# Performance work log

Measured on AMD Instinct MI355X. Metric: run time of the kernel, lower is better.

The kernel has to match this reference:

```python
import jax, jax.numpy as jnp
import numpy as np
from jax import lax

E = 4; D_MODEL = 128; D_FF = 128; DT_RANK = 32; D_STATE = 16
L = 12; PAD = 12  # padding_factor=1.0 -> pad L extra zeros
K_TOP = 6; U = 1e-6; EPS = 1e-5
BATCH = 8; NODES = 307; BN = BATCH * NODES
FREQ_IN = (L + PAD) // 2 + 1 + K_TOP  # 19
FREQ_OUT = L // 2 + 1                 # 7


def setup_inputs() -> dict:
    key = jax.random.key(0)
    ks = jax.random.split(key, 14)
    x = jax.random.normal(ks[0], (BN, L, D_MODEL), jnp.float32)
    graph = jax.random.normal(ks[1], (BATCH, L, D_FF, D_FF), jnp.float32) * (1.0 / D_FF)
    in_w = jax.random.normal(ks[2], (E, 2 * D_FF, D_MODEL), jnp.float32) * 0.05
    in_b = jax.random.normal(ks[3], (E, 2 * D_FF), jnp.float32) * 0.02
    x_w = jax.random.normal(ks[4], (E, DT_RANK + 2 * D_STATE + D_FF, D_FF), jnp.float32) * 0.05
    dt_w = jax.random.uniform(ks[5], (E, D_FF, DT_RANK), jnp.float32,
                              -(DT_RANK ** -0.5), DT_RANK ** -0.5)
    dt_b = -2.0 + 0.1 * jax.random.normal(ks[6], (E, D_FF), jnp.float32)
    A_log = jnp.broadcast_to(jnp.log(jnp.arange(1, D_STATE + 1, dtype=jnp.float32))[None, None, :],
                             (E, 1, D_STATE))
    out_w = jax.random.normal(ks[7], (E, D_MODEL, D_FF), jnp.float32) * 0.05
    out_b = jax.random.normal(ks[8], (E, D_MODEL), jnp.float32) * 0.02
    fw_r = jax.random.normal(ks[9], (E, FREQ_OUT, FREQ_IN), jnp.float32) * (FREQ_IN ** -0.5)
    fw_i = jax.random.normal(ks[10], (E, FREQ_OUT, FREQ_IN), jnp.float32) * (FREQ_IN ** -0.5)
    norm_w = jnp.ones((E, D_MODEL), jnp.float32)
    blk_w = jnp.full((E,), 0.5, jnp.float32)
    blk_b = jnp.full((E,), 0.5, jnp.float32)
    return dict(x=x, graph=graph, in_w=in_w, in_b=in_b, x_w=x_w, dt_w=dt_w, dt_b=dt_b,
                A_log=A_log, out_w=out_w, out_b=out_b, fw_r=fw_r, fw_i=fw_i,
                norm_w=norm_w, blk_w=blk_w, blk_b=blk_b)


def _rmsnorm(x, w):
    return x * lax.rsqrt(jnp.mean(x * x, axis=-1, keepdims=True) + EPS) * w


def _mamba_block(x, graph, in_w, in_b, x_w, dt_w, dt_b, A_log, out_w, out_b, fw_r, fw_i):
    bn, Ls, d = x.shape
    # --- FFT frequency gating ---
    x_padded = jnp.concatenate([x, jnp.zeros((bn, PAD, d), x.dtype)], axis=1)
    fp = jnp.fft.rfft(x_padded, axis=1)          # [bn, 13, d] complex
    f = jnp.fft.rfft(x, axis=1)                  # [bn, 7, d] complex
    sq_adj = (f.real + U) ** 2 + (f.imag + U) ** 2
    fs = -jnp.sort(-sq_adj, axis=1)[:, :K_TOP]   # top-K along freq dim, descending
    cat = jnp.concatenate([fp, fs.astype(fp.dtype)], axis=1)  # [bn, 19, d]
    W = lax.complex(fw_r, fw_i)                  # [7, 19]
    freq_proj = jnp.einsum('bkd,ok->bod', cat, W)  # [bn, 7, d]
    wf = jax.nn.softmax(freq_proj.real ** 2 + freq_proj.imag ** 2, axis=2)
    x_freq = jnp.fft.irfft(wf * f, axis=1)       # [bn, 12, d] (n = 2*(7-1))
    # --- input projection ---
    xz = x @ in_w.T + in_b
    xs, z = jnp.split(xz, 2, axis=-1)
    xs = jax.nn.silu(xs)
    # --- SSM ---
    A = -jnp.exp(A_log.astype(jnp.float32))      # [1, d_state]
    dbcd = xs @ x_w.T
    delta, B, C, Dp = jnp.split(dbcd, [DT_RANK, DT_RANK + D_STATE, DT_RANK + 2 * D_STATE], axis=-1)
    delta = jax.nn.softplus(delta @ dt_w.T + dt_b)  # [bn, L, d_ff]
    # graph mixing over nodes: bn = batch * n
    batch = graph.shape[0]
    delta = delta.reshape(batch, -1, Ls, D_FF)
    delta = jnp.einsum('bnsd,bsda->bnsa', delta, graph).reshape(bn, Ls, D_FF)
    deltaA = jnp.exp(delta[..., None] * A)             # [bn, L, d_ff, d_state]
    BX = delta[..., None] * B[:, :, None, :] * xs[..., None]
    dA_t = jnp.moveaxis(deltaA, 1, 0)
    bx_t = jnp.moveaxis(BX, 1, 0)

    def step(h, ab):
        dA, bx = ab
        h = dA * h + bx
        return h, h

    h0 = jnp.zeros((bn, D_FF, D_STATE), xs.dtype)
    _, hs = lax.scan(step, h0, (dA_t, bx_t))
    hs = jnp.moveaxis(hs, 0, 1)                        # [bn, L, d_ff, d_state]
    y = jnp.einsum('blds,bls->bld', hs, C) + Dp * xs
    # --- gate + output ---
    out = y * jax.nn.silu(z) * x_freq
    return out @ out_w.T + out_b


def reference(x, graph, in_w, in_b, x_w, dt_w, dt_b, A_log, out_w, out_b,
              fw_r, fw_i, norm_w, blk_w, blk_b):
    for i in range(E):
        xn = _rmsnorm(x, norm_w[i])
        out = _mamba_block(xn, graph, in_w[i], in_b[i], x_w[i], dt_w[i], dt_b[i],
                           A_log[i], out_w[i], out_b[i], fw_r[i], fw_i[i])
        out = blk_w[i] * out + blk_b[i]
        x = x + out  # dropout is identity in eval
    return jax.nn.silu(x)
```

## Files before the change

kernel.cpp:

```cpp
#include <hip/hip_runtime.h>
#include <math.h>

#define BN    2456
#define LSEQ  12
#define DM    128
#define NODES 307
#define MROWS 29472

typedef __bf16 bfx8 __attribute__((ext_vector_type(8)));
typedef float  f32x4 __attribute__((ext_vector_type(4)));

#define MFMA16(a, b, c) __builtin_amdgcn_mfma_f32_16x16x32_bf16(a, b, c, 0, 0, 0)

__device__ __forceinline__ float fsilu(float v)     { return v / (1.0f + __expf(-v)); }
__device__ __forceinline__ float fsoftplus(float x) { return fmaxf(x, 0.f) + __logf(1.0f + __expf(-fabsf(x))); }

__global__ __launch_bounds__(256)
void k_convert(const float* __restrict__ in_w, const float* __restrict__ x_w,
               const float* __restrict__ out_w, const float* __restrict__ dt_w,
               const float* __restrict__ graph,
               __bf16* __restrict__ in_w_bf, __bf16* __restrict__ x_w_bf,
               __bf16* __restrict__ out_w_bf, __bf16* __restrict__ dtw_bf,
               __bf16* __restrict__ graphT_bf) {
    int idx = blockIdx.x * 256 + threadIdx.x;
    if (idx < 131072) { in_w_bf[idx] = (__bf16)in_w[idx]; return; }
    idx -= 131072;
    if (idx < 98304) { x_w_bf[idx] = (__bf16)x_w[idx]; return; }
    idx -= 98304;
    if (idx < 65536) { out_w_bf[idx] = (__bf16)out_w[idx]; return; }
    idx -= 65536;
    if (idx < 65536) { dtw_bf[idx] = (__bf16)dt_w[idx]; return; }
    idx -= 65536;
    if (idx < 1572864) {
        int bl = idx >> 14, r = idx & 16383;
        int d = r >> 7, a = r & 127;
        graphT_bf[(size_t)bl * 16384 + a * 128 + d] = (__bf16)graph[idx];
    }
}

template <int N>
__device__ __forceinline__ void red_sum128(float* v, float* sred, int tid) {
#pragma unroll
    for (int off = 32; off; off >>= 1)
#pragma unroll
        for (int i = 0; i < N; ++i) v[i] += __shfl_xor(v[i], off, 64);
    if ((tid & 63) == 0) {
#pragma unroll
        for (int i = 0; i < N; ++i) sred[(tid >> 6) * N + i] = v[i];
    }
    __syncthreads();
#pragma unroll
    for (int i = 0; i < N; ++i) v[i] = sred[i] + sred[N + i];
    __syncthreads();
}

template <int N>
__device__ __forceinline__ void red_max128(float* v, float* sred, int tid) {
#pragma unroll
    for (int off = 32; off; off >>= 1)
#pragma unroll
        for (int i = 0; i < N; ++i) v[i] = fmaxf(v[i], __shfl_xor(v[i], off, 64));
    if ((tid & 63) == 0) {
#pragma unroll
        for (int i = 0; i < N; ++i) sred[(tid >> 6) * N + i] = v[i];
    }
    __syncthreads();
#pragma unroll
    for (int i = 0; i < N; ++i) v[i] = fmaxf(sred[i], sred[N + i]);
    __syncthreads();
}

__global__ __launch_bounds__(128)
void k_freq(const float* __restrict__ xcur, const float* __restrict__ norm_w,
            const float* __restrict__ fw_r, const float* __restrict__ fw_i,
            __bf16* __restrict__ xn_bf, __bf16* __restrict__ xfq_bf, int e) {
    __shared__ float s_c[24], s_s[24], s_wr[133], s_wi[133];
    __shared__ float sred[24];
    const int row = blockIdx.x, tid = threadIdx.x;
    const int b = row / NODES, n = row - b * NODES;

    if (tid < 24) {
        float sv, cv;
        __sincosf(6.283185307179586f * (float)tid / 24.0f, &sv, &cv);
        s_c[tid] = cv; s_s[tid] = sv;
    }
    for (int i = tid; i < 133; i += 128) { s_wr[i] = fw_r[e * 133 + i]; s_wi[i] = fw_i[e * 133 + i]; }

    const float* xp = xcur + (size_t)row * 1536 + tid;
    float xv[12], v[12];
#pragma unroll
    for (int l = 0; l < 12; ++l) { xv[l] = xp[l * 128]; v[l] = xv[l] * xv[l]; }
    __syncthreads();
    red_sum128<12>(v, sred, tid);

    const float nrmw = norm_w[e * DM + tid];
    float xnr[12];
#pragma unroll
    for (int l = 0; l < 12; ++l)
        xnr[l] = xv[l] * rsqrtf(v[l] * (1.0f / 128.0f) + 1e-5f) * nrmw;

#pragma unroll
    for (int l = 0; l < 12; ++l)
        xn_bf[((size_t)(b * 12 + l) * NODES + n) * 128 + tid] = (__bf16)xnr[l];

    float fpr[13], fpi[13];
#pragma unroll
    for (int k = 0; k < 13; ++k) { fpr[k] = 0.f; fpi[k] = 0.f; }
#pragma unroll
    for (int l = 0; l < 12; ++l) {
#pragma unroll
        for (int k = 0; k < 13; ++k) {
            const int t = (k * l) % 24;
            fpr[k] += xnr[l] * s_c[t];
            fpi[k] -= xnr[l] * s_s[t];
        }
    }

    float a7[7];
#pragma unroll
    for (int o2 = 0; o2 < 7; ++o2) {
        float ar = fpr[2 * o2] + 1e-6f, ai = fpi[2 * o2] + 1e-6f;
        a7[o2] = ar * ar + ai * ai;
    }
#pragma unroll
    for (int pss = 0; pss < 6; ++pss)
#pragma unroll
        for (int j = 0; j < 6; ++j) {
            float hi = fmaxf(a7[j], a7[j + 1]);
            float lo = fminf(a7[j], a7[j + 1]);
            a7[j] = hi; a7[j + 1] = lo;
        }

    float p7[7];
#pragma unroll
    for (int o2 = 0; o2 < 7; ++o2) {
        float pr = 0.f, pi = 0.f;
#pragma unroll
        for (int k = 0; k < 13; ++k) {
            const float wr = s_wr[o2 * 19 + k], wi = s_wi[o2 * 19 + k];
            pr += fpr[k] * wr - fpi[k] * wi;
            pi += fpr[k] * wi + fpi[k] * wr;
        }
#pragma unroll
        for (int k = 0; k < 6; ++k) {
            const float wr = s_wr[o2 * 19 + 13 + k], wi = s_wi[o2 * 19 + 13 + k];
            pr += a7[k] * wr;
            pi += a7[k] * wi;
        }
        p7[o2] = pr * pr + pi * pi;
    }

    float m7[7], ex[7], sm[7];
#pragma unroll
    for (int o2 = 0; o2 < 7; ++o2) m7[o2] = p7[o2];
    red_max128<7>(m7, sred, tid);
#pragma unroll
    for (int o2 = 0; o2 < 7; ++o2) { ex[o2] = __expf(p7[o2] - m7[o2]); sm[o2] = ex[o2]; }
    red_sum128<7>(sm, sred, tid);

    float gr[7], gi[7];
#pragma unroll
    for (int o2 = 0; o2 < 7; ++o2) {
        const float wf = ex[o2] / sm[o2];
        gr[o2] = wf * fpr[2 * o2];
        gi[o2] = wf * fpi[2 * o2];
    }

#pragma unroll
    for (int l = 0; l < 12; ++l) {
        float val = gr[0] + ((l & 1) ? -gr[6] : gr[6]);
#pragma unroll
        for (int o2 = 1; o2 < 6; ++o2) {
            const int t = (2 * o2 * l) % 24;
            val += 2.0f * (gr[o2] * s_c[t] - gi[o2] * s_s[t]);
        }
        xfq_bf[((size_t)(b * 12 + l) * NODES + n) * 128 + tid] = (__bf16)(val * (1.0f / 12.0f));
    }
}

__global__ __launch_bounds__(256)
void k_fused(const __bf16* __restrict__ xn_bf, const __bf16* __restrict__ in_w_bf,
             const float* __restrict__ in_b, const __bf16* __restrict__ x_w_bf,
             const __bf16* __restrict__ dtw_bf, const float* __restrict__ dt_b,
             const __bf16* __restrict__ graphT_bf,
             __bf16* __restrict__ xs_bf, __bf16* __restrict__ sz_bf,
             float* __restrict__ bcf32, __bf16* __restrict__ dpf,
             __bf16* __restrict__ dmix_bf, int e) {
    __shared__ __bf16 sxs[16 * 136];
    __shared__ __bf16 sdelta[16 * 136];
    __shared__ __bf16 sdel32[16 * 40];
    const int bl = blockIdx.x;
    const int n0 = blockIdx.y * 16;
    const int tid = threadIdx.x;
    const int wave = tid >> 6, lane = tid & 63;
    const int lm = lane & 15, lq = lane >> 4;
    const size_t rowbase = (size_t)bl * NODES + n0;

    const __bf16* Wi = in_w_bf + (size_t)e * 256 * 128;
    const size_t arow = (size_t)bl * NODES + min(n0 + lm, NODES - 1);
    bfx8 af[4];
#pragma unroll
    for (int kc = 0; kc < 4; ++kc)
        af[kc] = *(const bfx8*)(xn_bf + arow * 128 + kc * 32 + lq * 8);

    f32x4 acc[4];
#pragma unroll
    for (int nt = 0; nt < 4; ++nt) acc[nt] = (f32x4){0.f, 0.f, 0.f, 0.f};
#pragma unroll
    for (int kc = 0; kc < 4; ++kc) {
        const int kb = kc * 32 + lq * 8;
#pragma unroll
        for (int ntl = 0; ntl < 4; ++ntl) {
            bfx8 b = *(const bfx8*)(Wi + (size_t)(wave * 64 + ntl * 16 + lm) * 128 + kb);
            acc[ntl] = MFMA16(af[kc], b, acc[ntl]);
        }
    }
#pragma unroll
    for (int ntl = 0; ntl < 4; ++ntl) {
        const int col = wave * 64 + ntl * 16 + lm;
        const float bias = in_b[e * 256 + col];
#pragma unroll
        for (int r = 0; r < 4; ++r) {
            const int node = lq * 4 + r;
            const float v = fsilu(acc[ntl][r] + bias);
            const int ok = (n0 + node) < NODES;
            if (col < 128) {
                sxs[node * 136 + col] = (__bf16)v;
                if (ok) xs_bf[(rowbase + node) * 128 + col] = (__bf16)v;
            } else if (ok) {
                sz_bf[(rowbase + node) * 128 + (col - 128)] = (__bf16)v;
            }
        }
    }
    __syncthreads();

    const __bf16* Wx = x_w_bf + (size_t)e * 192 * 128;
    bfx8 ax[4];
#pragma unroll
    for (int kc = 0; kc < 4; ++kc)
        ax[kc] = *(const bfx8*)(sxs + lm * 136 + kc * 32 + lq * 8);

    f32x4 xacc[3];
#pragma unroll
    for (int nt = 0; nt < 3; ++nt) xacc[nt] = (f32x4){0.f, 0.f, 0.f, 0.f};
#pragma unroll
    for (int kc = 0; kc < 4; ++kc) {
        const int kb = kc * 32 + lq * 8;
#pragma unroll
        for (int ntl = 0; ntl < 3; ++ntl) {
            bfx8 b = *(const bfx8*)(Wx + (size_t)((wave * 3 + ntl) * 16 + lm) * 128 + kb);
            xacc[ntl] = MFMA16(ax[kc], b, xacc[ntl]);
        }
    }
#pragma unroll
    for (int ntl = 0; ntl < 3; ++ntl) {
        const int col = (wave * 3 + ntl) * 16 + lm;
#pragma unroll
        for (int r = 0; r < 4; ++r) {
            const int node = lq * 4 + r;
            const float v = xacc[ntl][r];
            const int ok = (n0 + node) < NODES;
            if (col < 32) sdel32[node * 40 + col] = (__bf16)v;
            else if (col < 64) { if (ok) bcf32[(rowbase + node) * 32 + (col - 32)] = v; }
            else if (ok) dpf[(rowbase + node) * 128 + (col - 64)] = (__bf16)v;
        }
    }
    __syncthreads();

    const __bf16* DW = dtw_bf + (size_t)e * 128 * 32;
    bfx8 ad = *(const bfx8*)(sdel32 + lm * 40 + lq * 8);
    const f32x4 z4 = {0.f, 0.f, 0.f, 0.f};
#pragma unroll
    for (int ntl = 0; ntl < 2; ++ntl) {
        const int nt = wave * 2 + ntl;
        bfx8 b = *(const bfx8*)(DW + (size_t)(nt * 16 + lm) * 32 + lq * 8);
        f32x4 dacc = MFMA16(ad, b, z4);
        const int col = nt * 16 + lm;
        const float bias = dt_b[e * 128 + col];
#pragma unroll
        for (int r = 0; r < 4; ++r) {
            const int node = lq * 4 + r;
            sdelta[node * 136 + col] = (__bf16)fsoftplus(dacc[r] + bias);
        }
    }
    __syncthreads();

    const __bf16* Gp = graphT_bf + (size_t)bl * 16384;
    bfx8 ag[4];
#pragma unroll
    for (int kc = 0; kc < 4; ++kc)
        ag[kc] = *(const bfx8*)(sdelta + lm * 136 + kc * 32 + lq * 8);

#pragma unroll
    for (int ntl = 0; ntl < 2; ++ntl) {
        const int nt = wave * 2 + ntl;
        f32x4 gacc = z4;
#pragma unroll
        for (int kc = 0; kc < 4; ++kc) {
            const int kb = kc * 32 + lq * 8;
            bfx8 b = *(const bfx8*)(Gp + (size_t)(nt * 16 + lm) * 128 + kb);
            gacc = MFMA16(ag[kc], b, gacc);
        }
        const int col = nt * 16 + lm;
#pragma unroll
        for (int r = 0; r < 4; ++r) {
            const int node = lq * 4 + r;
            if ((n0 + node) < NODES)
                dmix_bf[(rowbase + node) * 128 + col] = (__bf16)gacc[r];
        }
    }
}

__global__ __launch_bounds__(128)
void k_scanout(const __bf16* __restrict__ dmix_bf, const __bf16* __restrict__ xs_bf,
               const __bf16* __restrict__ sz_bf, const __bf16* __restrict__ xfq_bf,
               const float* __restrict__ bcf32, const __bf16* __restrict__ dpf,
               const float* __restrict__ A_log, const __bf16* __restrict__ out_w_bf,
               const float* __restrict__ out_b, const float* __restrict__ blk_w,
               const float* __restrict__ blk_b, const float* __restrict__ xprev,
               float* __restrict__ xout, int e, int last) {
    __shared__ __bf16 s_out[16 * 136];
    __shared__ float sBC[384];
    const int row = blockIdx.x, tid = threadIdx.x;
    const int b = row / NODES, n = row - b * NODES;
    for (int i = tid; i < 384; i += 128) {
        const int l = i >> 5, s = i & 31;
        sBC[i] = bcf32[((size_t)(b * 12 + l) * NODES + n) * 32 + s];
    }
    float As[16];
#pragma unroll
    for (int s = 0; s < 16; ++s) As[s] = -__expf(A_log[e * 16 + s]);
#pragma unroll
    for (int r = 12; r < 16; ++r) s_out[r * 136 + tid] = (__bf16)0.f;
    __syncthreads();

    float h[16];
#pragma unroll
    for (int s = 0; s < 16; ++s) h[s] = 0.f;
#pragma unroll
    for (int l = 0; l < 12; ++l) {
        const size_t base = ((size_t)(b * 12 + l) * NODES + n) * 128 + tid;
        const float dl = (float)dmix_bf[base];
        const float xv = (float)xs_bf[base];
        const float Dp = (float)dpf[base];
        const float dlx = dl * xv;
        float y = 0.f;
#pragma unroll
        for (int s = 0; s < 16; ++s) {
            h[s] = __expf(dl * As[s]) * h[s] + sBC[l * 32 + s] * dlx;
            y += h[s] * sBC[l * 32 + 16 + s];
        }
        y += Dp * xv;
        const float g = y * (float)sz_bf[base] * (float)xfq_bf[base];
        s_out[l * 136 + tid] = (__bf16)g;
    }
    __syncthreads();

    const int wave = tid >> 6, lane = tid & 63;
    const int lm = lane & 15, lq = lane >> 4;
    const __bf16* Wo = out_w_bf + (size_t)e * 16384;
    bfx8 a[4];
#pragma unroll
    for (int kc = 0; kc < 4; ++kc)
        a[kc] = *(const bfx8*)(s_out + lm * 136 + kc * 32 + lq * 8);

    f32x4 acc[4];
#pragma unroll
    for (int nt = 0; nt < 4; ++nt) acc[nt] = (f32x4){0.f, 0.f, 0.f, 0.f};
#pragma unroll
    for (int kc = 0; kc < 4; ++kc) {
        const int kb = kc * 32 + lq * 8;
#pragma unroll
        for (int nt = 0; nt < 4; ++nt) {
            bfx8 b = *(const bfx8*)(Wo + (size_t)(wave * 64 + nt * 16 + lm) * 128 + kb);
            acc[nt] = MFMA16(a[kc], b, acc[nt]);
        }
    }

    const float bw = blk_w[e], bb = blk_b[e];
#pragma unroll
    for (int nt = 0; nt < 4; ++nt) {
        const int col = wave * 64 + nt * 16 + lm;
        const float ob = out_b[e * 128 + col];
#pragma unroll
        for (int r = 0; r < 4; ++r) {
            const int m = lq * 4 + r;
            if (m < 12) {
                const size_t gi = ((size_t)row * 12 + m) * 128 + col;
                float v = bw * (acc[nt][r] + ob) + bb + xprev[gi];
                if (last) v = fsilu(v);
                xout[gi] = v;
            }
        }
    }
}

extern "C" void kernel_launch(void* const* d_in, const int* in_sizes, int n_in,
                              void* d_out, int out_size, void* d_ws, size_t ws_size,
                              hipStream_t stream) {
    (void)in_sizes; (void)n_in; (void)out_size; (void)ws_size;
    const float* x_in   = (const float*)d_in[0];
    const float* graph  = (const float*)d_in[1];
    const float* in_w   = (const float*)d_in[2];
    const float* in_b   = (const float*)d_in[3];
    const float* x_w    = (const float*)d_in[4];
    const float* dt_w   = (const float*)d_in[5];
    const float* dt_b   = (const float*)d_in[6];
    const float* A_log  = (const float*)d_in[7];
    const float* out_w  = (const float*)d_in[8];
    const float* out_b  = (const float*)d_in[9];
    const float* fw_r   = (const float*)d_in[10];
    const float* fw_i   = (const float*)d_in[11];
    const float* norm_w = (const float*)d_in[12];
    const float* blk_w  = (const float*)d_in[13];
    const float* blk_b  = (const float*)d_in[14];
    float* out = (float*)d_out;

    float* ws = (float*)d_ws;
    size_t o = 0;
    __bf16* in_w_bf   = (__bf16*)(ws + o); o += 131072 / 2;
    __bf16* x_w_bf    = (__bf16*)(ws + o); o += 98304 / 2;
    __bf16* out_w_bf  = (__bf16*)(ws + o); o += 65536 / 2;
    __bf16* dtw_bf    = (__bf16*)(ws + o); o += 65536 / 2;
    __bf16* graphT_bf = (__bf16*)(ws + o); o += 1572864 / 2;
    const size_t NE = (size_t)MROWS * 128;
    __bf16* xn_bf    = (__bf16*)(ws + o); o += NE / 2;
    __bf16* xfq_bf   = (__bf16*)(ws + o); o += NE / 2;
    __bf16* xs_bf    = (__bf16*)(ws + o); o += NE / 2;
    __bf16* sz_bf    = (__bf16*)(ws + o); o += NE / 2;
    __bf16* dpf      = (__bf16*)(ws + o); o += NE / 2;
    __bf16* dmix_bf  = (__bf16*)(ws + o); o += NE / 2;
    float*  bcf32    = ws + o;            o += (size_t)MROWS * 32;

    hipLaunchKernelGGL(k_convert, dim3(7552), dim3(256), 0, stream,
                       in_w, x_w, out_w, dt_w, graph,
                       in_w_bf, x_w_bf, out_w_bf, dtw_bf, graphT_bf);

    for (int e = 0; e < 4; ++e) {
        const float* xcur = (e == 0) ? x_in : (const float*)out;
        const int last = (e == 3) ? 1 : 0;
        hipLaunchKernelGGL(k_freq, dim3(BN), dim3(128), 0, stream,
                           xcur, norm_w, fw_r, fw_i, xn_bf, xfq_bf, e);
        hipLaunchKernelGGL(k_fused, dim3(96, 20), dim3(256), 0, stream,
                           xn_bf, in_w_bf, in_b, x_w_bf, dtw_bf, dt_b, graphT_bf,
                           xs_bf, sz_bf, bcf32, dpf, dmix_bf, e);
        hipLaunchKernelGGL(k_scanout, dim3(BN), dim3(128), 0, stream,
                           dmix_bf, xs_bf, sz_bf, xfq_bf, bcf32, dpf, A_log,
                           out_w_bf, out_b, blk_w, blk_b, xcur, out, e, last);
    }
}
```

Baseline: 467.3 us.

## Fuse next expert's RMSNorm and frequency gating into the scan/output kernel epilogue

New measurement: 483.4 us. +3.4%, slower.

```diff
diff --git a/kernel.cpp b/kernel.cpp
--- a/kernel.cpp
+++ b/kernel.cpp
@@ -70,12 +70,107 @@
     __syncthreads();
 }
 
+__device__ __forceinline__
+void freq_body(const float* __restrict__ s_res, const float* __restrict__ norm_w,
+               float* s_c, float* s_s, float* s_wr, float* s_wi, float* sred,
+               __bf16* __restrict__ xn_bf, __bf16* __restrict__ xfq_bf,
+               int b, int n, int e, int tid) {
+    float xv[12], v[12];
+#pragma unroll
+    for (int l = 0; l < 12; ++l) { xv[l] = s_res[l * 132 + tid]; v[l] = xv[l] * xv[l]; }
+    red_sum128<12>(v, sred, tid);
+
+    const float nrmw = norm_w[e * DM + tid];
+    float xnr[12];
+#pragma unroll
+    for (int l = 0; l < 12; ++l)
+        xnr[l] = xv[l] * rsqrtf(v[l] * (1.0f / 128.0f) + 1e-5f) * nrmw;
+
+#pragma unroll
+    for (int l = 0; l < 12; ++l)
+        xn_bf[((size_t)(b * 12 + l) * NODES + n) * 128 + tid] = (__bf16)xnr[l];
+
+    float fpr[13], fpi[13];
+#pragma unroll
+    for (int k = 0; k < 13; ++k) { fpr[k] = 0.f; fpi[k] = 0.f; }
+#pragma unroll
+    for (int l = 0; l < 12; ++l) {
+#pragma unroll
+        for (int k = 0; k < 13; ++k) {
+            const int t = (k * l) % 24;
+            fpr[k] += xnr[l] * s_c[t];
+            fpi[k] -= xnr[l] * s_s[t];
+        }
+    }
+
+    float a7[7];
+#pragma unroll
+    for (int o2 = 0; o2 < 7; ++o2) {
+        float ar = fpr[2 * o2] + 1e-6f, ai = fpi[2 * o2] + 1e-6f;
+        a7[o2] = ar * ar + ai * ai;
+    }
+#pragma unroll
+    for (int pss = 0; pss < 6; ++pss)
+#pragma unroll
+        for (int j = 0; j < 6; ++j) {
+            float hi = fmaxf(a7[j], a7[j + 1]);
+            float lo = fminf(a7[j], a7[j + 1]);
+            a7[j] = hi; a7[j + 1] = lo;
+        }
+
+    float p7[7];
+#pragma unroll
+    for (int o2 = 0; o2 < 7; ++o2) {
+        float pr = 0.f, pi = 0.f;
+#pragma unroll
+        for (int k = 0; k < 13; ++k) {
+            const float wr = s_wr[o2 * 19 + k], wi = s_wi[o2 * 19 + k];
+            pr += fpr[k] * wr - fpi[k] * wi;
+            pi += fpr[k] * wi + fpi[k] * wr;
+        }
+#pragma unroll
+        for (int k = 0; k < 6; ++k) {
+            const float wr = s_wr[o2 * 19 + 13 + k], wi = s_wi[o2 * 19 + 13 + k];
+            pr += a7[k] * wr;
+            pi += a7[k] * wi;
+        }
+        p7[o2] = pr * pr + pi * pi;
+    }
+
+    float m7[7], ex[7], sm[7];
+#pragma unroll
+    for (int o2 = 0; o2 < 7; ++o2) m7[o2] = p7[o2];
+    red_max128<7>(m7, sred, tid);
+#pragma unroll
+    for (int o2 = 0; o2 < 7; ++o2) { ex[o2] = __expf(p7[o2] - m7[o2]); sm[o2] = ex[o2]; }
+    red_sum128<7>(sm, sred, tid);
+
+    float gr[7], gi[7];
+#pragma unroll
+    for (int o2 = 0; o2 < 7; ++o2) {
+        const float wf = ex[o2] / sm[o2];
+        gr[o2] = wf * fpr[2 * o2];
+        gi[o2] = wf * fpi[2 * o2];
+    }
+
+#pragma unroll
+    for (int l = 0; l < 12; ++l) {
+        float val = gr[0] + ((l & 1) ? -gr[6] : gr[6]);
+#pragma unroll
+        for (int o2 = 1; o2 < 6; ++o2) {
+            const int t = (2 * o2 * l) % 24;
+            val += 2.0f * (gr[o2] * s_c[t] - gi[o2] * s_s[t]);
+        }
+        xfq_bf[((size_t)(b * 12 + l) * NODES + n) * 128 + tid] = (__bf16)(val * (1.0f / 12.0f));
+    }
+}
+
 __global__ __launch_bounds__(128)
 void k_freq(const float* __restrict__ xcur, const float* __restrict__ norm_w,
             const float* __restrict__ fw_r, const float* __restrict__ fw_i,
             __bf16* __restrict__ xn_bf, __bf16* __restrict__ xfq_bf, int e) {
-    __shared__ float s_c[24], s_s[24], s_wr[133], s_wi[133];
-    __shared__ float sred[24];
+    __shared__ float s_res[12 * 132];
+    __shared__ float s_c[24], s_s[24], s_wr[133], s_wi[133], sred[24];
     const int row = blockIdx.x, tid = threadIdx.x;
     const int b = row / NODES, n = row - b * NODES;
 
@@ -85,97 +180,11 @@
         s_c[tid] = cv; s_s[tid] = sv;
     }
     for (int i = tid; i < 133; i += 128) { s_wr[i] = fw_r[e * 133 + i]; s_wi[i] = fw_i[e * 133 + i]; }
-
     const float* xp = xcur + (size_t)row * 1536 + tid;
-    float xv[12], v[12];
-#pragma unroll
-    for (int l = 0; l < 12; ++l) { xv[l] = xp[l * 128]; v[l] = xv[l] * xv[l]; }
-    __syncthreads();
-    red_sum128<12>(v, sred, tid);
-
-    const float nrmw = norm_w[e * DM + tid];
-    float xnr[12];
-#pragma unroll
-    for (int l = 0; l < 12; ++l)
-        xnr[l] = xv[l] * rsqrtf(v[l] * (1.0f / 128.0f) + 1e-5f) * nrmw;
-
-#pragma unroll
-    for (int l = 0; l < 12; ++l)
-        xn_bf[((size_t)(b * 12 + l) * NODES + n) * 128 + tid] = (__bf16)xnr[l];
-
-    float fpr[13], fpi[13];
-#pragma unroll
-    for (int k = 0; k < 13; ++k) { fpr[k] = 0.f; fpi[k] = 0.f; }
-#pragma unroll
-    for (int l = 0; l < 12; ++l) {
-#pragma unroll
-        for (int k = 0; k < 13; ++k) {
-            const int t = (k * l) % 24;
-            fpr[k] += xnr[l] * s_c[t];
-            fpi[k] -= xnr[l] * s_s[t];
-        }
-    }
-
-    float a7[7];
-#pragma unroll
-    for (int o2 = 0; o2 < 7; ++o2) {
-        float ar = fpr[2 * o2] + 1e-6f, ai = fpi[2 * o2] + 1e-6f;
-        a7[o2] = ar * ar + ai * ai;
-    }
-#pragma unroll
-    for (int pss = 0; pss < 6; ++pss)
-#pragma unroll
-        for (int j = 0; j < 6; ++j) {
-            float hi = fmaxf(a7[j], a7[j + 1]);
-            float lo = fminf(a7[j], a7[j + 1]);
-            a7[j] = hi; a7[j + 1] = lo;
-        }
-
-    float p7[7];
-#pragma unroll
-    for (int o2 = 0; o2 < 7; ++o2) {
-        float pr = 0.f, pi = 0.f;
-#pragma unroll
-        for (int k = 0; k < 13; ++k) {
-            const float wr = s_wr[o2 * 19 + k], wi = s_wi[o2 * 19 + k];
-            pr += fpr[k] * wr - fpi[k] * wi;
-            pi += fpr[k] * wi + fpi[k] * wr;
-        }
-#pragma unroll
-        for (int k = 0; k < 6; ++k) {
-            const float wr = s_wr[o2 * 19 + 13 + k], wi = s_wi[o2 * 19 + 13 + k];
-            pr += a7[k] * wr;
-            pi += a7[k] * wi;
-        }
-        p7[o2] = pr * pr + pi * pi;
-    }
-
-    float m7[7], ex[7], sm[7];
-#pragma unroll
-    for (int o2 = 0; o2 < 7; ++o2) m7[o2] = p7[o2];
-    red_max128<7>(m7, sred, tid);
-#pragma unroll
-    for (int o2 = 0; o2 < 7; ++o2) { ex[o2] = __expf(p7[o2] - m7[o2]); sm[o2] = ex[o2]; }
-    red_sum128<7>(sm, sred, tid);
-
-    float gr[7], gi[7];
-#pragma unroll
-    for (int o2 = 0; o2 < 7; ++o2) {
-        const float wf = ex[o2] / sm[o2];
-        gr[o2] = wf * fpr[2 * o2];
-        gi[o2] = wf * fpi[2 * o2];
-    }
-
-#pragma unroll
-    for (int l = 0; l < 12; ++l) {
-        float val = gr[0] + ((l & 1) ? -gr[6] : gr[6]);
-#pragma unroll
-        for (int o2 = 1; o2 < 6; ++o2) {
-            const int t = (2 * o2 * l) % 24;
-            val += 2.0f * (gr[o2] * s_c[t] - gi[o2] * s_s[t]);
-        }
-        xfq_bf[((size_t)(b * 12 + l) * NODES + n) * 128 + tid] = (__bf16)(val * (1.0f / 12.0f));
-    }
+#pragma unroll
+    for (int l = 0; l < 12; ++l) s_res[l * 132 + tid] = xp[l * 128];
+    __syncthreads();
+    freq_body(s_res, norm_w, s_c, s_s, s_wr, s_wi, sred, xn_bf, xfq_bf, b, n, e, tid);
 }
 
 __global__ __launch_bounds__(256)
@@ -318,11 +327,27 @@
                const float* __restrict__ A_log, const __bf16* __restrict__ out_w_bf,
                const float* __restrict__ out_b, const float* __restrict__ blk_w,
                const float* __restrict__ blk_b, const float* __restrict__ xprev,
-               float* __restrict__ xout, int e, int last) {
+               float* __restrict__ xout,
+               const float* __restrict__ norm_w, const float* __restrict__ fw_r,
+               const float* __restrict__ fw_i, __bf16* __restrict__ xn_bf,
+               __bf16* __restrict__ xfq_out, int e, int last) {
     __shared__ __bf16 s_out[16 * 136];
     __shared__ float sBC[384];
+    __shared__ float s_res[12 * 132];
+    __shared__ float s_c[24], s_s[24], s_wr[133], s_wi[133], sred[24];
     const int row = blockIdx.x, tid = threadIdx.x;
     const int b = row / NODES, n = row - b * NODES;
+
+    if (tid < 24) {
+        float sv, cv;
+        __sincosf(6.283185307179586f * (float)tid / 24.0f, &sv, &cv);
+        s_c[tid] = cv; s_s[tid] = sv;
+    }
+    if (!last)
+        for (int i = tid; i < 133; i += 128) {
+            s_wr[i] = fw_r[(e + 1) * 133 + i];
+            s_wi[i] = fw_i[(e + 1) * 133 + i];
+        }
     for (int i = tid; i < 384; i += 128) {
         const int l = i >> 5, s = i & 31;
         sBC[i] = bcf32[((size_t)(b * 12 + l) * NODES + n) * 32 + s];
@@ -372,8 +397,8 @@
         const int kb = kc * 32 + lq * 8;
 #pragma unroll
         for (int nt = 0; nt < 4; ++nt) {
-            bfx8 b = *(const bfx8*)(Wo + (size_t)(wave * 64 + nt * 16 + lm) * 128 + kb);
-            acc[nt] = MFMA16(a[kc], b, acc[nt]);
+            bfx8 bw8 = *(const bfx8*)(Wo + (size_t)(wave * 64 + nt * 16 + lm) * 128 + kb);
+            acc[nt] = MFMA16(a[kc], bw8, acc[nt]);
         }
     }
 
@@ -390,8 +415,15 @@
                 float v = bw * (acc[nt][r] + ob) + bb + xprev[gi];
                 if (last) v = fsilu(v);
                 xout[gi] = v;
+                s_res[m * 132 + col] = v;
             }
         }
+    }
+
+    if (!last) {
+        __syncthreads();
+        freq_body(s_res, norm_w, s_c, s_s, s_wr, s_wi, sred,
+                  xn_bf, xfq_out, b, n, e + 1, tid);
     }
 }
 
@@ -436,16 +468,18 @@
                        in_w, x_w, out_w, dt_w, graph,
                        in_w_bf, x_w_bf, out_w_bf, dtw_bf, graphT_bf);
 
+    hipLaunchKernelGGL(k_freq, dim3(BN), dim3(128), 0, stream,
+                       x_in, norm_w, fw_r, fw_i, xn_bf, xfq_bf, 0);
+
     for (int e = 0; e < 4; ++e) {
         const float* xcur = (e == 0) ? x_in : (const float*)out;
         const int last = (e == 3) ? 1 : 0;
-        hipLaunchKernelGGL(k_freq, dim3(BN), dim3(128), 0, stream,
-                           xcur, norm_w, fw_r, fw_i, xn_bf, xfq_bf, e);
         hipLaunchKernelGGL(k_fused, dim3(96, 20), dim3(256), 0, stream,
                            xn_bf, in_w_bf, in_b, x_w_bf, dtw_bf, dt_b, graphT_bf,
                            xs_bf, sz_bf, bcf32, dpf, dmix_bf, e);
         hipLaunchKernelGGL(k_scanout, dim3(BN), dim3(128), 0, stream,
                            dmix_bf, xs_bf, sz_bf, xfq_bf, bcf32, dpf, A_log,
-                           out_w_bf, out_b, blk_w, blk_b, xcur, out, e, last);
-    }
-}
+                           out_w_bf, out_b, blk_w, blk_b, xcur, out,
+                           norm_w, fw_r, fw_i, xn_bf, xfq_bf, e, last);
+    }
+}
```
